# Performance work log

Measured on AMD Instinct MI355X. Metric: run time of the kernel, lower is better.

Reference implementation:

```python
import jax, jax.numpy as jnp
import numpy as np


def setup_inputs() -> dict:
    key = jax.random.key(0)
    k1, k2 = jax.random.split(key)
    B, S, HOP, L = 32, 524288, 256, 100
    frames = S // HOP
    # input hook asserts 0 <= phase <= 0.5
    wrapped_phase = jax.random.uniform(k1, (B, S), dtype=jnp.float32) * 0.5
    tables = jax.random.normal(k2, (B, frames + 1, L), dtype=jnp.float32)
    return {"wrapped_phase": wrapped_phase, "tables": tables, "hop_length": HOP}


def reference(wrapped_phase, tables, hop_length):
    # wrapped_phase: (B, S), hop_length divides S; tables: (B, S//hop + 1, L)
    B, S = wrapped_phase.shape
    frames = S // hop_length
    L = tables.shape[2]

    wp = wrapped_phase.reshape(B, frames, hop_length)          # (B, F, H)
    idx_raw = wp * L
    floor_idx = jnp.clip(idx_raw.astype(jnp.int32), 0, L - 1)  # (B, F, H)
    p = idx_raw - floor_idx.astype(wp.dtype)                   # frac along table axis

    # wrap-around pad of one sample along table axis: (B, F+1, L+1)
    padded = jnp.concatenate([tables, tables[:, :, :1]], axis=2)
    floor_flow = padded[:, :-1]                                # (B, F, L+1) frame t
    ceil_flow = padded[:, 1:]                                  # (B, F, L+1) frame t+1

    def lerp_table(flow):
        lo = jnp.take_along_axis(flow, floor_idx, axis=2)
        hi = jnp.take_along_axis(flow, floor_idx + 1, axis=2)
        return lo * (1 - p) + hi * p

    sel_floor = lerp_table(floor_flow)                         # (B, F, H)
    sel_ceil = lerp_table(ceil_flow)

    # interpolate across hop (frame) dimension
    p2 = jnp.arange(hop_length, dtype=wp.dtype) / hop_length   # (H,)
    final = sel_floor * (1 - p2) + sel_ceil * p2
    return final.reshape(B, -1)[:, :S]
```

## Files before the change

kernel.cpp:

```cpp
#include <hip/hip_runtime.h>

constexpr int HOP    = 256;
constexpr int L      = 100;
constexpr int FRAMES = 2048;
constexpr int B      = 32;
constexpr int FPB    = 4;
constexpr int GPR    = FRAMES / FPB;
constexpr int GROUPS = B * GPR;
constexpr int GPBLK  = 8;
constexpr int NBLK   = GROUPS / GPBLK;

constexpr int TABF   = (FPB + 1) * L;

typedef const __attribute__((address_space(1))) void gvoid;
typedef __attribute__((address_space(3)))       void svoid;

__global__ __launch_bounds__(256) void glottal_kernel(
    const float* __restrict__ wp,
    const float* __restrict__ tables,
    float* __restrict__ out)
{
    __shared__ float tab[2][TABF];

    const int tid  = threadIdx.x;
    const int wv   = tid >> 6;
    const int lane = tid & 63;
    const int grp0 = blockIdx.x * GPBLK;

    const float4* wp4  = reinterpret_cast<const float4*>(wp);
    float4*       out4 = reinterpret_cast<float4*>(out);

    auto stage_tab = [&](int g, int pp) {
        if (tid < TABF / 4) {
            const int b = g >> 9;
            const int r = g & (GPR - 1);
            const float* src = tables
                + ((size_t)b * (FRAMES + 1) + (size_t)r * FPB) * L + tid * 4;
            __builtin_amdgcn_global_load_lds((gvoid*)src,
                                             (svoid*)&tab[pp][tid * 4], 16, 0, 0);
        }
    };

    stage_tab(grp0, 0);
    float4 wnext = wp4[(size_t)grp0 * 256 + tid];
    __syncthreads();

    for (int it = 0; it < GPBLK; ++it) {
        const int pp  = it & 1;
        const int grp = grp0 + it;
        const float4 w = wnext;

        if (it + 1 < GPBLK) {
            wnext = wp4[(size_t)(grp + 1) * 256 + tid];
            stage_tab(grp + 1, pp ^ 1);
        }

        const float* trow = &tab[pp][wv * L];
        const float  wv4[4] = {w.x, w.y, w.z, w.w};
        const float  p2b = (float)(lane * 4) * (1.0f / HOP);
        float res[4];
#pragma unroll
        for (int k = 0; k < 4; ++k) {
            const float ir = wv4[k] * (float)L;
            int fi = (int)ir;
            fi = fi > L - 1 ? L - 1 : fi;
            const float p   = ir - (float)fi;
            const float lo0 = trow[fi],     lo1 = trow[fi + 1];
            const float hi0 = trow[fi + L], hi1 = trow[fi + L + 1];
            const float sf  = lo0 + (lo1 - lo0) * p;
            const float sc  = hi0 + (hi1 - hi0) * p;
            res[k] = sf + (sc - sf) * (p2b + (float)k * (1.0f / HOP));
        }

        out4[(size_t)grp * 256 + tid] = make_float4(res[0], res[1], res[2], res[3]);

        __syncthreads();
    }
}

extern "C" void kernel_launch(void* const* d_in, const int* in_sizes, int n_in,
                              void* d_out, int out_size, void* d_ws, size_t ws_size,
                              hipStream_t stream) {
    const float* wp     = (const float*)d_in[0];
    const float* tables = (const float*)d_in[1];
    float* out = (float*)d_out;

    dim3 grid(NBLK);
    glottal_kernel<<<grid, 256, 0, stream>>>(wp, tables, out);
}
```

Measured before the change: 137.1 us.

## Give each wave private frame rows and drop block-wide barriers

Replaces the block-shared, async-staged 4-frame table tile with a per-wave double-buffered LDS copy of the two table rows each frame needs. Each wave now handles 8 consecutive frames on its own. It prefetches the next rows and phases into registers, so the per-iteration __syncthreads goes away. The cost is reloading each table row twice, once as the current frame and once as the next, plus an explicit wrap index for the top table entry.

```diff
diff --git a/kernel.cpp b/kernel.cpp
--- a/kernel.cpp
+++ b/kernel.cpp
@@ -4,60 +4,51 @@
 constexpr int L      = 100;
 constexpr int FRAMES = 2048;
 constexpr int B      = 32;
-constexpr int FPB    = 4;
-constexpr int GPR    = FRAMES / FPB;
-constexpr int GROUPS = B * GPR;
-constexpr int GPBLK  = 8;
-constexpr int NBLK   = GROUPS / GPBLK;
-
-constexpr int TABF   = (FPB + 1) * L;
-
-typedef const __attribute__((address_space(1))) void gvoid;
-typedef __attribute__((address_space(3)))       void svoid;
+constexpr int FPW    = 8;
+constexpr int TOTF   = B * FRAMES;
+constexpr int NWAVE  = TOTF / FPW;
+constexpr int NBLK   = NWAVE / 4;
 
 __global__ __launch_bounds__(256) void glottal_kernel(
     const float* __restrict__ wp,
     const float* __restrict__ tables,
     float* __restrict__ out)
 {
-    __shared__ float tab[2][TABF];
+    __shared__ float priv[4][2][2 * L];
 
     const int tid  = threadIdx.x;
     const int wv   = tid >> 6;
     const int lane = tid & 63;
-    const int grp0 = blockIdx.x * GPBLK;
+    const int f0   = (blockIdx.x * 4 + wv) * FPW;
 
-    const float4* wp4  = reinterpret_cast<const float4*>(wp);
-    float4*       out4 = reinterpret_cast<float4*>(out);
+    float (*pv)[2 * L] = priv[wv];
 
-    auto stage_tab = [&](int g, int pp) {
-        if (tid < TABF / 4) {
-            const int b = g >> 9;
-            const int r = g & (GPR - 1);
-            const float* src = tables
-                + ((size_t)b * (FRAMES + 1) + (size_t)r * FPB) * L + tid * 4;
-            __builtin_amdgcn_global_load_lds((gvoid*)src,
-                                             (svoid*)&tab[pp][tid * 4], 16, 0, 0);
-        }
+    auto row_ptr = [&](int f) {
+        const int b = f >> 11;
+        const int r = f & (FRAMES - 1);
+        return tables + ((size_t)b * (FRAMES + 1) + (size_t)r) * L;
     };
 
-    stage_tab(grp0, 0);
-    float4 wnext = wp4[(size_t)grp0 * 256 + tid];
-    __syncthreads();
+    float4 rcur = make_float4(0.f, 0.f, 0.f, 0.f);
+    if (lane < 50)
+        rcur = *reinterpret_cast<const float4*>(row_ptr(f0) + lane * 4);
+    float4 wcur = *reinterpret_cast<const float4*>(wp + (size_t)f0 * HOP + lane * 4);
+    if (lane < 50)
+        *reinterpret_cast<float4*>(&pv[0][lane * 4]) = rcur;
 
-    for (int it = 0; it < GPBLK; ++it) {
-        const int pp  = it & 1;
-        const int grp = grp0 + it;
-        const float4 w = wnext;
+    float4 rnxt, wnxt;
+    for (int it = 0; it < FPW; ++it) {
+        const int f  = f0 + it;
+        const int pp = it & 1;
 
-        if (it + 1 < GPBLK) {
-            wnext = wp4[(size_t)(grp + 1) * 256 + tid];
-            stage_tab(grp + 1, pp ^ 1);
+        if (it + 1 < FPW) {
+            if (lane < 50)
+                rnxt = *reinterpret_cast<const float4*>(row_ptr(f + 1) + lane * 4);
+            wnxt = *reinterpret_cast<const float4*>(wp + (size_t)(f + 1) * HOP + lane * 4);
         }
 
-        const float* trow = &tab[pp][wv * L];
-        const float  wv4[4] = {w.x, w.y, w.z, w.w};
-        const float  p2b = (float)(lane * 4) * (1.0f / HOP);
+        const float* t = pv[pp];
+        const float  wv4[4] = {wcur.x, wcur.y, wcur.z, wcur.w};
         float res[4];
 #pragma unroll
         for (int k = 0; k < 4; ++k) {
@@ -65,16 +56,23 @@
             int fi = (int)ir;
             fi = fi > L - 1 ? L - 1 : fi;
             const float p   = ir - (float)fi;
-            const float lo0 = trow[fi],     lo1 = trow[fi + 1];
-            const float hi0 = trow[fi + L], hi1 = trow[fi + L + 1];
+            const int   ihi = (fi + 1 == L) ? 0 : fi + 1;
+            const float lo0 = t[fi],       cl0 = t[fi + L];
+            const float lo1 = t[ihi],      cl1 = t[ihi + L];
             const float sf  = lo0 + (lo1 - lo0) * p;
-            const float sc  = hi0 + (hi1 - hi0) * p;
-            res[k] = sf + (sc - sf) * (p2b + (float)k * (1.0f / HOP));
+            const float sc  = cl0 + (cl1 - cl0) * p;
+            const float p2  = (float)(lane * 4 + k) * (1.0f / HOP);
+            res[k] = sf + (sc - sf) * p2;
         }
 
-        out4[(size_t)grp * 256 + tid] = make_float4(res[0], res[1], res[2], res[3]);
+        *reinterpret_cast<float4*>(out + (size_t)f * HOP + lane * 4) =
+            make_float4(res[0], res[1], res[2], res[3]);
 
-        __syncthreads();
+        if (it + 1 < FPW) {
+            if (lane < 50)
+                *reinterpret_cast<float4*>(&pv[pp ^ 1][lane * 4]) = rnxt;
+            wcur = wnxt;
+        }
     }
 }
 
```

New measurement: 137.4 us. No clear change (+0.3%).
